# Kernel tuning notes

Measured on AMD Instinct MI355X. Metric: run time of the kernel, lower is better.

The kernel has to match this reference:

```python
import jax, jax.numpy as jnp
import numpy as np

EPS = 1e-8
N, C, R = 512, 32, 32


def _eijk():
    e = np.zeros((3, 3, 3), np.float32)
    e[0, 1, 2] = e[1, 2, 0] = e[2, 0, 1] = 1.0
    e[0, 2, 1] = e[2, 1, 0] = e[1, 0, 2] = -1.0
    return jnp.asarray(e)


def _unit(v):
    # unit_vectors: v / (|v| + EPS)
    return v / (jnp.linalg.norm(v, axis=-1, keepdims=True) + EPS)


def _y2(r):
    # real l=2 spherical harmonics (TFN convention), [N,N,5]
    x, y, z = r[..., 0], r[..., 1], r[..., 2]
    r2 = jnp.maximum(jnp.sum(r * r, axis=-1), EPS)
    c = float(2.0 * np.sqrt(3.0))
    return jnp.stack([
        x * y / r2,
        y * z / r2,
        (-x * x - y * y + 2.0 * z * z) / (c * r2),
        z * x / r2,
        (x * x - y * y) / (2.0 * r2),
    ], axis=-1)


def _forward(in0, in1, in2, rbf, rij,
             w1_f00, b1_f00, w2_f00, b2_f00,
             w1_f01, b1_f01, w2_f01, b2_f01,
             w1_f02, b1_f02, w2_f02, b2_f02,
             w1_f10, b1_f10, w2_f10, b2_f10,
             w1_f11, b1_f11, w2_f11, b2_f11):
    def rad(w1, b1, w2, b2):
        # RadialFunction: relu(b1 + rbf @ w1^T) @ w2^T + b2 -> [N,N,C]
        h = jax.nn.relu(b1 + jnp.einsum('abr,hr->abh', rbf, w1))
        return b2 + jnp.einsum('abh,ch->abc', h, w2)

    # mask self/zero-distance pairs (dij < EPS -> radial = 0), as in F_1/F_2
    mask = (jnp.linalg.norm(rij, axis=-1) >= EPS).astype(rbf.dtype)[..., None]  # [N,N,1]
    u = _unit(rij)    # [N,N,3]
    y2 = _y2(rij)     # [N,N,5]

    r00 = rad(w1_f00, b1_f00, w2_f00, b2_f00)            # scalar filter F_0
    r01 = rad(w1_f01, b1_f01, w2_f01, b2_f01) * mask     # F_1 radial, 0x1->1
    r02 = rad(w1_f02, b1_f02, w2_f02, b2_f02) * mask     # F_2 radial, 0x2->2
    r10 = rad(w1_f10, b1_f10, w2_f10, b2_f10) * mask     # F_1 radial, 1x1->0
    r11 = rad(w1_f11, b1_f11, w2_f11, b2_f11) * mask     # F_1 radial, 1x1->1

    # Filter_0_output_0 (identity CG): L x 0 -> L, aggregate over neighbors b
    o0_s = jnp.einsum('abf,bfi->afi', r00, in0)          # [N,C,1]
    o1_s = jnp.einsum('abf,bfi->afi', r00, in1)          # [N,C,3]
    o2_s = jnp.einsum('abf,bfi->afi', r00, in2)          # [N,C,5]
    o1_a = jnp.einsum('abi,abf,bf->afi', u, r01, in0[..., 0])
    o2_a = jnp.einsum('abi,abf,bf->afi', y2, r02, in0[..., 0])
    o0_b = jnp.einsum('abj,abf,bfj->af', u, r10, in1)[..., None]
    o1_c = jnp.einsum('ijk,abj,abf,bfk->afi', _eijk(), u, r11, in1)

    return (jnp.stack([o0_s, o0_b]),          # [2,N,C,1]
            jnp.stack([o1_a, o1_s, o1_c]),    # [3,N,C,3]
            jnp.stack([o2_a, o2_s]))          # [2,N,C,5]


def setup_inputs() -> dict:
    key = jax.random.key(0)
    ks = jax.random.split(key, 16)

    def xav(k, shape):
        lim = float(np.sqrt(6.0 / (shape[0] + shape[1])))
        return jax.random.uniform(k, shape, jnp.float32, -lim, lim)

    pos = jax.random.normal(ks[0], (N, 3), jnp.float32) * 3.0
    rij = pos[:, None, :] - pos[None, :, :]  # [N,N,3]; zero diagonal exercises the dij<EPS mask
    inp = {
        'in0': jax.random.normal(ks[1], (N, C, 1), jnp.float32),
        'in1': jax.random.normal(ks[2], (N, C, 3), jnp.float32),
        'in2': jax.random.normal(ks[3], (N, C, 5), jnp.float32),
        'rbf': jax.random.uniform(ks[4], (N, N, R), jnp.float32),
        'rij': rij,
    }
    for i, n in enumerate(['f00', 'f01', 'f02', 'f10', 'f11']):
        inp['w1_' + n] = xav(ks[5 + 2 * i], (R, R))
        inp['b1_' + n] = jnp.zeros((R,), jnp.float32)
        inp['w2_' + n] = xav(ks[6 + 2 * i], (C, R))
        inp['b2_' + n] = jnp.zeros((C,), jnp.float32)
    return inp


def reference(in0, in1, in2, rbf, rij,
              w1_f00, b1_f00, w2_f00, b2_f00,
              w1_f01, b1_f01, w2_f01, b2_f01,
              w1_f02, b1_f02, w2_f02, b2_f02,
              w1_f10, b1_f10, w2_f10, b2_f10,
              w1_f11, b1_f11, w2_f11, b2_f11):
    return _forward(in0, in1, in2, rbf, rij,
                    w1_f00, b1_f00, w2_f00, b2_f00,
                    w1_f01, b1_f01, w2_f01, b2_f01,
                    w1_f02, b1_f02, w2_f02, b2_f02,
                    w1_f10, b1_f10, w2_f10, b2_f10,
                    w1_f11, b1_f11, w2_f11, b2_f11)
```

## Files before the change

kernel.cpp:

```cpp
#include <hip/hip_runtime.h>
#include <math.h>

#define NN 512
#define CC 32
#define EPSF 1e-8f
#define WS 40
#define GS 12

typedef __attribute__((ext_vector_type(8))) short bf16x8;
typedef __attribute__((ext_vector_type(4))) float f32x4;

__device__ __forceinline__ short f2bf(float f) {
    unsigned u = __float_as_uint(f);
    u += 0x7fffu + ((u >> 16) & 1u);
    return (short)(u >> 16);
}

__device__ __forceinline__ unsigned cvtpk(float lo, float hi) {
    unsigned r;
    asm("v_cvt_pk_bf16_f32 %0, %1, %2" : "=v"(r) : "v"(lo), "v"(hi));
    return r;
}

#define STAGE_F(F, W1P, W2P)                                                   \
    {                                                                          \
        wlds[(((F) * 2 + 0) * 32 + n0) * WS + k0]      = f2bf((W1P)[tid]);     \
        wlds[(((F) * 2 + 0) * 32 + n0 + 16) * WS + k0] = f2bf((W1P)[tid+512]); \
        wlds[(((F) * 2 + 1) * 32 + n0) * WS + k2]      = f2bf((W2P)[tid]);     \
        wlds[(((F) * 2 + 1) * 32 + n0 + 16) * WS + k2] = f2bf((W2P)[tid+512]); \
    }

#define MLP3S(WOFF, BOFF, B2V, R)                                                  \
    {                                                                              \
        const bf16x8 w1loM = *(const bf16x8*)&wlds[(WOFF) + ln * WS + q * 8];      \
        const bf16x8 w1hiM = *(const bf16x8*)&wlds[(WOFF) + (16 + ln) * WS + q * 8]; \
        f32x4 d0M = *(const f32x4*)&b1lds[(BOFF) + 4 * q];                         \
        f32x4 d1M = *(const f32x4*)&b1lds[(BOFF) + 16 + 4 * q];                    \
        d0M = __builtin_amdgcn_mfma_f32_16x16x32_bf16(w1loM, rbfF, d0M, 0, 0, 0);  \
        d1M = __builtin_amdgcn_mfma_f32_16x16x32_bf16(w1hiM, rbfF, d1M, 0, 0, 0);  \
        union { bf16x8 v; unsigned u[4]; } hu;                                     \
        hu.u[0] = cvtpk(fmaxf(d0M[0], 0.f), fmaxf(d0M[1], 0.f));                   \
        hu.u[1] = cvtpk(fmaxf(d0M[2], 0.f), fmaxf(d0M[3], 0.f));                   \
        hu.u[2] = cvtpk(fmaxf(d1M[0], 0.f), fmaxf(d1M[1], 0.f));                   \
        hu.u[3] = cvtpk(fmaxf(d1M[2], 0.f), fmaxf(d1M[3], 0.f));                   \
        const bf16x8 w2M = *(const bf16x8*)&wlds[(WOFF) + (32 + ch0 + ln) * WS + q * 8]; \
        f32x4 eM = { (B2V), (B2V), (B2V), (B2V) };                                 \
        R = __builtin_amdgcn_mfma_f32_16x16x32_bf16(hu.v, w2M, eM, 0, 0, 0);       \
    }

#define AGGM(RR)                                                               \
    {                                                                          \
        const int bA = b0 + q * 4 + (RR);                                      \
        const f32x4 gA = *(const f32x4*)&geomall[bA][0];                       \
        const f32x4 gB = *(const f32x4*)&geomall[bA][4];                       \
        const float i0A = in0[bA * CC + cw];                                   \
        const float* i1A = in1 + (bA * CC + cw) * 3;                           \
        const float x1A = i1A[0], y1A = i1A[1], z1A = i1A[2];                  \
        const float* i2A = in2 + (bA * CC + cw) * 5;                           \
        const float p0A = i2A[0], p1A = i2A[1], p2A = i2A[2];                  \
        const float p3A = i2A[3], p4A = i2A[4];                                \
        const float s0A = rF0[(RR)];                                           \
        a0  = fmaf(s0A, i0A, a0);                                              \
        a5  = fmaf(s0A, x1A, a5);                                              \
        a6  = fmaf(s0A, y1A, a6);                                              \
        a7  = fmaf(s0A, z1A, a7);                                              \
        a16 = fmaf(s0A, p0A, a16);                                             \
        a17 = fmaf(s0A, p1A, a17);                                             \
        a18 = fmaf(s0A, p2A, a18);                                             \
        a19 = fmaf(s0A, p3A, a19);                                             \
        a20 = fmaf(s0A, p4A, a20);                                             \
        const float t1A = rF1[(RR)] * i0A;                                     \
        a2  = fmaf(t1A, gA[0], a2);                                            \
        a3  = fmaf(t1A, gA[1], a3);                                            \
        a4  = fmaf(t1A, gA[2], a4);                                            \
        const float t2A = rF2[(RR)] * i0A;                                     \
        a11 = fmaf(t2A, gA[3], a11);                                           \
        a12 = fmaf(t2A, gB[0], a12);                                           \
        a13 = fmaf(t2A, gB[1], a13);                                           \
        a14 = fmaf(t2A, gB[2], a14);                                           \
        a15 = fmaf(t2A, gB[3], a15);                                           \
        const float dtA = fmaf(gA[2], z1A, fmaf(gA[1], y1A, gA[0] * x1A));     \
        a1  = fmaf(rF3[(RR)], dtA, a1);                                        \
        const float cxA = fmaf(gA[1], z1A, -(gA[2] * y1A));                    \
        const float cyA = fmaf(gA[2], x1A, -(gA[0] * z1A));                    \
        const float czA = fmaf(gA[0], y1A, -(gA[1] * x1A));                    \
        a8  = fmaf(rF4[(RR)], cxA, a8);                                        \
        a9  = fmaf(rF4[(RR)], cyA, a9);                                        \
        a10 = fmaf(rF4[(RR)], czA, a10);                                       \
    }

#define RED(CMP, V)                                                            \
    {                                                                          \
        float vR = (V);                                                        \
        vR += __shfl_down(vR, 32);                                             \
        vR += __shfl_down(vR, 16);                                             \
        if (lane < 16) red[(w * 21 + (CMP)) * 16 + ln] = vR;                   \
    }

__global__ __launch_bounds__(512, 3) void tfn_mfma(
    const float* __restrict__ in0,
    const float* __restrict__ in1,
    const float* __restrict__ in2,
    const float* __restrict__ rbf,
    const float* __restrict__ rij,
    const float* __restrict__ w1_0, const float* __restrict__ b1_0,
    const float* __restrict__ w2_0, const float* __restrict__ b2_0,
    const float* __restrict__ w1_1, const float* __restrict__ b1_1,
    const float* __restrict__ w2_1, const float* __restrict__ b2_1,
    const float* __restrict__ w1_2, const float* __restrict__ b1_2,
    const float* __restrict__ w2_2, const float* __restrict__ b2_2,
    const float* __restrict__ w1_3, const float* __restrict__ b1_3,
    const float* __restrict__ w2_3, const float* __restrict__ b2_3,
    const float* __restrict__ w1_4, const float* __restrict__ b1_4,
    const float* __restrict__ w2_4, const float* __restrict__ b2_4,
    float* __restrict__ out)
{
    const int a    = blockIdx.x;
    const int tid  = threadIdx.x;
    const int w    = tid >> 6;
    const int lane = tid & 63;
    const int q    = lane >> 4;
    const int ln   = lane & 15;
    const int ch0  = (w & 1) * 16;
    const int cw   = ch0 + ln;

    __shared__ short wlds[5 * 2 * 32 * WS];
    __shared__ float geomall[NN][GS];
    __shared__ float b1lds[5 * 32];

    const int n0 = tid >> 5, k0 = tid & 31;
    const int k2 = (k0 < 16) ? ((k0 >> 2) * 8 + (k0 & 3))
                             : (((k0 - 16) >> 2) * 8 + 4 + ((k0 - 16) & 3));

    STAGE_F(0, w1_0, w2_0)
    STAGE_F(1, w1_1, w2_1)
    STAGE_F(2, w1_2, w2_2)
    STAGE_F(3, w1_3, w2_3)
    STAGE_F(4, w1_4, w2_4)

    if (tid < 32) {
        b1lds[0 * 32 + tid] = b1_0[tid];
        b1lds[1 * 32 + tid] = b1_1[tid];
        b1lds[2 * 32 + tid] = b1_2[tid];
        b1lds[3 * 32 + tid] = b1_3[tid];
        b1lds[4 * 32 + tid] = b1_4[tid];
    }

    const size_t rowbase = (size_t)a * NN;
    const float Y2C = 0.28867513459481287f;

    {
        const float* rp = rij + (rowbase + tid) * 3;
        const float x = rp[0], y = rp[1], z = rp[2];
        const float d2 = x * x + y * y + z * z;
        const float d  = sqrtf(d2);
        const float m  = (d >= EPSF) ? 1.f : 0.f;
        const float inv = m / (d + EPSF);
        const float ir2 = m / fmaxf(d2, EPSF);
        f32x4 gA = { x * inv, y * inv, z * inv, x * y * ir2 };
        f32x4 gB = { y * z * ir2, (2.f * z * z - x * x - y * y) * (ir2 * Y2C),
                     z * x * ir2, (x * x - y * y) * (ir2 * 0.5f) };
        *(f32x4*)&geomall[tid][0] = gA;
        *(f32x4*)&geomall[tid][4] = gB;
    }

    const float b2v0 = b2_0[cw], b2v1 = b2_1[cw], b2v2 = b2_2[cw];
    const float b2v3 = b2_3[cw], b2v4 = b2_4[cw];
    __syncthreads();

    float a0 = 0.f, a1 = 0.f, a2 = 0.f, a3 = 0.f, a4 = 0.f, a5 = 0.f, a6 = 0.f;
    float a7 = 0.f, a8 = 0.f, a9 = 0.f, a10 = 0.f, a11 = 0.f, a12 = 0.f, a13 = 0.f;
    float a14 = 0.f, a15 = 0.f, a16 = 0.f, a17 = 0.f, a18 = 0.f, a19 = 0.f, a20 = 0.f;

    const int pairb = (w >> 1) * 128;
    const float* rbase = rbf + (rowbase + pairb + ln) * 32 + q * 8;

    f32x4 curA = *(const f32x4*)rbase;
    f32x4 curB = *(const f32x4*)(rbase + 4);

    #pragma unroll 1
    for (int t = 0; t < 8; ++t) {
        const int b0 = pairb + t * 16;

        union { bf16x8 v; unsigned u[4]; } ru;
        ru.u[0] = cvtpk(curA[0], curA[1]);
        ru.u[1] = cvtpk(curA[2], curA[3]);
        ru.u[2] = cvtpk(curB[0], curB[1]);
        ru.u[3] = cvtpk(curB[2], curB[3]);
        const bf16x8 rbfF = ru.v;
        if (t < 7) {
            curA = *(const f32x4*)(rbase + (t + 1) * 512);
            curB = *(const f32x4*)(rbase + (t + 1) * 512 + 4);
        }

        f32x4 rF0, rF1, rF2, rF3, rF4;
        MLP3S(0 * 64 * WS, 0 * 32, b2v0, rF0)
        MLP3S(1 * 64 * WS, 1 * 32, b2v1, rF1)
        MLP3S(2 * 64 * WS, 2 * 32, b2v2, rF2)
        MLP3S(3 * 64 * WS, 3 * 32, b2v3, rF3)
        MLP3S(4 * 64 * WS, 4 * 32, b2v4, rF4)

        AGGM(0) AGGM(1) AGGM(2) AGGM(3)
    }

    __syncthreads();
    float* red = (float*)wlds;
    RED(0,  a0)  RED(1,  a1)  RED(2,  a2)  RED(3,  a3)  RED(4,  a4)
    RED(5,  a5)  RED(6,  a6)  RED(7,  a7)  RED(8,  a8)  RED(9,  a9)
    RED(10, a10) RED(11, a11) RED(12, a12) RED(13, a13) RED(14, a14)
    RED(15, a15) RED(16, a16) RED(17, a17) RED(18, a18) RED(19, a19)
    RED(20, a20)
    __syncthreads();

    const int NC = NN * CC;
    for (int e = tid; e < 21 * 32; e += 512) {
        const int cmp = e >> 5, c = e & 31;
        const int hh = c >> 4, l2 = c & 15;
        float s = 0.f;
        #pragma unroll
        for (int p = 0; p < 4; ++p)
            s += red[((p * 2 + hh) * 21 + cmp) * 16 + l2];
        int idx;
        if (cmp == 0)       idx = a * CC + c;
        else if (cmp == 1)  idx = NC + a * CC + c;
        else if (cmp < 5)   idx = 2 * NC + (a * CC + c) * 3 + (cmp - 2);
        else if (cmp < 8)   idx = 2 * NC + 3 * NC + (a * CC + c) * 3 + (cmp - 5);
        else if (cmp < 11)  idx = 2 * NC + 6 * NC + (a * CC + c) * 3 + (cmp - 8);
        else if (cmp < 16)  idx = 11 * NC + (a * CC + c) * 5 + (cmp - 11);
        else                idx = 11 * NC + 5 * NC + (a * CC + c) * 5 + (cmp - 16);
        out[idx] = s;
    }
}

extern "C" void kernel_launch(void* const* d_in, const int* in_sizes, int n_in,
                              void* d_out, int out_size, void* d_ws, size_t ws_size,
                              hipStream_t stream) {
    const float* in0 = (const float*)d_in[0];
    const float* in1 = (const float*)d_in[1];
    const float* in2 = (const float*)d_in[2];
    const float* rbf = (const float*)d_in[3];
    const float* rij = (const float*)d_in[4];

    hipLaunchKernelGGL(tfn_mfma, dim3(NN), dim3(512), 0, stream,
                       in0, in1, in2, rbf, rij,
                       (const float*)d_in[5],  (const float*)d_in[6],
                       (const float*)d_in[7],  (const float*)d_in[8],
                       (const float*)d_in[9],  (const float*)d_in[10],
                       (const float*)d_in[11], (const float*)d_in[12],
                       (const float*)d_in[13], (const float*)d_in[14],
                       (const float*)d_in[15], (const float*)d_in[16],
                       (const float*)d_in[17], (const float*)d_in[18],
                       (const float*)d_in[19], (const float*)d_in[20],
                       (const float*)d_in[21], (const float*)d_in[22],
                       (const float*)d_in[23], (const float*)d_in[24],
                       (float*)d_out);
}
```

Measured before the change: 40.28 us.

## Software-pipeline MFMA radial MLP with aggregation using double-buffered filter registers

Result: slower. 98.15 us (+143.6%).

```diff
diff --git a/kernel.cpp b/kernel.cpp
--- a/kernel.cpp
+++ b/kernel.cpp
@@ -48,7 +48,26 @@
         R = __builtin_amdgcn_mfma_f32_16x16x32_bf16(hu.v, w2M, eM, 0, 0, 0);       \
     }
 
-#define AGGM(RR)                                                               \
+#define MLP_GROUP(NEXT_T, DO_PF, R0, R1, R2, R3, R4)                           \
+    {                                                                          \
+        union { bf16x8 v; unsigned u[4]; } ru;                                 \
+        ru.u[0] = cvtpk(pfA[0], pfA[1]);                                       \
+        ru.u[1] = cvtpk(pfA[2], pfA[3]);                                       \
+        ru.u[2] = cvtpk(pfB[0], pfB[1]);                                       \
+        ru.u[3] = cvtpk(pfB[2], pfB[3]);                                       \
+        const bf16x8 rbfF = ru.v;                                              \
+        if (DO_PF) {                                                           \
+            pfA = *(const f32x4*)(rbase + (NEXT_T) * 512);                     \
+            pfB = *(const f32x4*)(rbase + (NEXT_T) * 512 + 4);                 \
+        }                                                                      \
+        MLP3S(0 * 64 * WS, 0 * 32, b2v0, R0)                                   \
+        MLP3S(1 * 64 * WS, 1 * 32, b2v1, R1)                                   \
+        MLP3S(2 * 64 * WS, 2 * 32, b2v2, R2)                                   \
+        MLP3S(3 * 64 * WS, 3 * 32, b2v3, R3)                                   \
+        MLP3S(4 * 64 * WS, 4 * 32, b2v4, R4)                                   \
+    }
+
+#define AGGM(RR, S0, S1, S2, S3, S4)                                           \
     {                                                                          \
         const int bA = b0 + q * 4 + (RR);                                      \
         const f32x4 gA = *(const f32x4*)&geomall[bA][0];                       \
@@ -59,7 +78,7 @@
         const float* i2A = in2 + (bA * CC + cw) * 5;                           \
         const float p0A = i2A[0], p1A = i2A[1], p2A = i2A[2];                  \
         const float p3A = i2A[3], p4A = i2A[4];                                \
-        const float s0A = rF0[(RR)];                                           \
+        const float s0A = S0[(RR)];                                            \
         a0  = fmaf(s0A, i0A, a0);                                              \
         a5  = fmaf(s0A, x1A, a5);                                              \
         a6  = fmaf(s0A, y1A, a6);                                              \
@@ -69,24 +88,33 @@
         a18 = fmaf(s0A, p2A, a18);                                             \
         a19 = fmaf(s0A, p3A, a19);                                             \
         a20 = fmaf(s0A, p4A, a20);                                             \
-        const float t1A = rF1[(RR)] * i0A;                                     \
+        const float t1A = S1[(RR)] * i0A;                                      \
         a2  = fmaf(t1A, gA[0], a2);                                            \
         a3  = fmaf(t1A, gA[1], a3);                                            \
         a4  = fmaf(t1A, gA[2], a4);                                            \
-        const float t2A = rF2[(RR)] * i0A;                                     \
+        const float t2A = S2[(RR)] * i0A;                                      \
         a11 = fmaf(t2A, gA[3], a11);                                           \
         a12 = fmaf(t2A, gB[0], a12);                                           \
         a13 = fmaf(t2A, gB[1], a13);                                           \
         a14 = fmaf(t2A, gB[2], a14);                                           \
         a15 = fmaf(t2A, gB[3], a15);                                           \
         const float dtA = fmaf(gA[2], z1A, fmaf(gA[1], y1A, gA[0] * x1A));     \
-        a1  = fmaf(rF3[(RR)], dtA, a1);                                        \
+        a1  = fmaf(S3[(RR)], dtA, a1);                                         \
         const float cxA = fmaf(gA[1], z1A, -(gA[2] * y1A));                    \
         const float cyA = fmaf(gA[2], x1A, -(gA[0] * z1A));                    \
         const float czA = fmaf(gA[0], y1A, -(gA[1] * x1A));                    \
-        a8  = fmaf(rF4[(RR)], cxA, a8);                                        \
-        a9  = fmaf(rF4[(RR)], cyA, a9);                                        \
-        a10 = fmaf(rF4[(RR)], czA, a10);                                       \
+        a8  = fmaf(S4[(RR)], cxA, a8);                                         \
+        a9  = fmaf(S4[(RR)], cyA, a9);                                         \
+        a10 = fmaf(S4[(RR)], czA, a10);                                        \
+    }
+
+#define AGGM4(T, S0, S1, S2, S3, S4)                                           \
+    {                                                                          \
+        const int b0 = pairb + (T) * 16;                                       \
+        AGGM(0, S0, S1, S2, S3, S4)                                            \
+        AGGM(1, S0, S1, S2, S3, S4)                                            \
+        AGGM(2, S0, S1, S2, S3, S4)                                            \
+        AGGM(3, S0, S1, S2, S3, S4)                                            \
     }
 
 #define RED(CMP, V)                                                            \
@@ -97,7 +125,7 @@
         if (lane < 16) red[(w * 21 + (CMP)) * 16 + ln] = vR;                   \
     }
 
-__global__ __launch_bounds__(512, 3) void tfn_mfma(
+__global__ __launch_bounds__(512, 2) void tfn_mfma(
     const float* __restrict__ in0,
     const float* __restrict__ in1,
     const float* __restrict__ in2,
@@ -175,33 +203,22 @@
     const int pairb = (w >> 1) * 128;
     const float* rbase = rbf + (rowbase + pairb + ln) * 32 + q * 8;
 
-    f32x4 curA = *(const f32x4*)rbase;
-    f32x4 curB = *(const f32x4*)(rbase + 4);
+    f32x4 pfA = *(const f32x4*)rbase;
+    f32x4 pfB = *(const f32x4*)(rbase + 4);
+    f32x4 rA0, rA1, rA2, rA3, rA4, rB0, rB1, rB2, rB3, rB4;
+
+    MLP_GROUP(1, 1, rA0, rA1, rA2, rA3, rA4)
 
     #pragma unroll 1
-    for (int t = 0; t < 8; ++t) {
-        const int b0 = pairb + t * 16;
-
-        union { bf16x8 v; unsigned u[4]; } ru;
-        ru.u[0] = cvtpk(curA[0], curA[1]);
-        ru.u[1] = cvtpk(curA[2], curA[3]);
-        ru.u[2] = cvtpk(curB[0], curB[1]);
-        ru.u[3] = cvtpk(curB[2], curB[3]);
-        const bf16x8 rbfF = ru.v;
-        if (t < 7) {
-            curA = *(const f32x4*)(rbase + (t + 1) * 512);
-            curB = *(const f32x4*)(rbase + (t + 1) * 512 + 4);
-        }
-
-        f32x4 rF0, rF1, rF2, rF3, rF4;
-        MLP3S(0 * 64 * WS, 0 * 32, b2v0, rF0)
-        MLP3S(1 * 64 * WS, 1 * 32, b2v1, rF1)
-        MLP3S(2 * 64 * WS, 2 * 32, b2v2, rF2)
-        MLP3S(3 * 64 * WS, 3 * 32, b2v3, rF3)
-        MLP3S(4 * 64 * WS, 4 * 32, b2v4, rF4)
-
-        AGGM(0) AGGM(1) AGGM(2) AGGM(3)
-    }
+    for (int tt = 0; tt < 3; ++tt) {
+        MLP_GROUP(2 * tt + 2, 1, rB0, rB1, rB2, rB3, rB4)
+        AGGM4(2 * tt,     rA0, rA1, rA2, rA3, rA4)
+        MLP_GROUP(2 * tt + 3, 1, rA0, rA1, rA2, rA3, rA4)
+        AGGM4(2 * tt + 1, rB0, rB1, rB2, rB3, rB4)
+    }
+    MLP_GROUP(0, 0, rB0, rB1, rB2, rB3, rB4)
+    AGGM4(6, rA0, rA1, rA2, rA3, rA4)
+    AGGM4(7, rB0, rB1, rB2, rB3, rB4)
 
     __syncthreads();
     float* red = (float*)wlds;
```

## Switch radial MLPs to 32x32x16 MFMA covering all channels per wave

Applied to the files above, without the earlier changes.

After: 91.35 us. 2.27x slower.

```diff
diff --git a/kernel.cpp b/kernel.cpp
--- a/kernel.cpp
+++ b/kernel.cpp
@@ -9,6 +9,7 @@
 
 typedef __attribute__((ext_vector_type(8))) short bf16x8;
 typedef __attribute__((ext_vector_type(4))) float f32x4;
+typedef __attribute__((ext_vector_type(16))) float f32x16;
 
 __device__ __forceinline__ short f2bf(float f) {
     unsigned u = __float_as_uint(f);
@@ -30,74 +31,91 @@
         wlds[(((F) * 2 + 1) * 32 + n0 + 16) * WS + k2] = f2bf((W2P)[tid+512]); \
     }
 
-#define MLP3S(WOFF, BOFF, B2V, R)                                                  \
+#define LAYER12(F, B2V, RAD)                                                       \
     {                                                                              \
-        const bf16x8 w1loM = *(const bf16x8*)&wlds[(WOFF) + ln * WS + q * 8];      \
-        const bf16x8 w1hiM = *(const bf16x8*)&wlds[(WOFF) + (16 + ln) * WS + q * 8]; \
-        f32x4 d0M = *(const f32x4*)&b1lds[(BOFF) + 4 * q];                         \
-        f32x4 d1M = *(const f32x4*)&b1lds[(BOFF) + 16 + 4 * q];                    \
-        d0M = __builtin_amdgcn_mfma_f32_16x16x32_bf16(w1loM, rbfF, d0M, 0, 0, 0);  \
-        d1M = __builtin_amdgcn_mfma_f32_16x16x32_bf16(w1hiM, rbfF, d1M, 0, 0, 0);  \
-        union { bf16x8 v; unsigned u[4]; } hu;                                     \
-        hu.u[0] = cvtpk(fmaxf(d0M[0], 0.f), fmaxf(d0M[1], 0.f));                   \
-        hu.u[1] = cvtpk(fmaxf(d0M[2], 0.f), fmaxf(d0M[3], 0.f));                   \
-        hu.u[2] = cvtpk(fmaxf(d1M[0], 0.f), fmaxf(d1M[1], 0.f));                   \
-        hu.u[3] = cvtpk(fmaxf(d1M[2], 0.f), fmaxf(d1M[3], 0.f));                   \
-        const bf16x8 w2M = *(const bf16x8*)&wlds[(WOFF) + (32 + ch0 + ln) * WS + q * 8]; \
-        f32x4 eM = { (B2V), (B2V), (B2V), (B2V) };                                 \
-        R = __builtin_amdgcn_mfma_f32_16x16x32_bf16(hu.v, w2M, eM, 0, 0, 0);       \
-    }
-
-#define AGGM(RR)                                                               \
-    {                                                                          \
-        const int bA = b0 + q * 4 + (RR);                                      \
-        const f32x4 gA = *(const f32x4*)&geomall[bA][0];                       \
-        const f32x4 gB = *(const f32x4*)&geomall[bA][4];                       \
-        const float i0A = in0[bA * CC + cw];                                   \
-        const float* i1A = in1 + (bA * CC + cw) * 3;                           \
-        const float x1A = i1A[0], y1A = i1A[1], z1A = i1A[2];                  \
-        const float* i2A = in2 + (bA * CC + cw) * 5;                           \
-        const float p0A = i2A[0], p1A = i2A[1], p2A = i2A[2];                  \
-        const float p3A = i2A[3], p4A = i2A[4];                                \
-        const float s0A = rF0[(RR)];                                           \
-        a0  = fmaf(s0A, i0A, a0);                                              \
-        a5  = fmaf(s0A, x1A, a5);                                              \
-        a6  = fmaf(s0A, y1A, a6);                                              \
-        a7  = fmaf(s0A, z1A, a7);                                              \
-        a16 = fmaf(s0A, p0A, a16);                                             \
-        a17 = fmaf(s0A, p1A, a17);                                             \
-        a18 = fmaf(s0A, p2A, a18);                                             \
-        a19 = fmaf(s0A, p3A, a19);                                             \
-        a20 = fmaf(s0A, p4A, a20);                                             \
-        const float t1A = rF1[(RR)] * i0A;                                     \
+        const bf16x8 w1i0M = *(const bf16x8*)&wlds[(((F)*2+0)*32 + cc)*WS + 8*hp]; \
+        const bf16x8 w1i1M = *(const bf16x8*)&wlds[(((F)*2+0)*32 + cc)*WS + 16 + 8*hp]; \
+        f32x16 d1M = *(const f32x16*)&b1p[(F)*32 + hp*16];                         \
+        d1M = __builtin_amdgcn_mfma_f32_32x32x16_bf16(w1i0M, rbf0F, d1M, 0, 0, 0); \
+        d1M = __builtin_amdgcn_mfma_f32_32x32x16_bf16(w1i1M, rbf1F, d1M, 0, 0, 0); \
+        union { bf16x8 v; unsigned u[4]; } hAM, hBM;                               \
+        hAM.u[0] = cvtpk(fmaxf(d1M[0],  0.f), fmaxf(d1M[1],  0.f));                \
+        hAM.u[1] = cvtpk(fmaxf(d1M[2],  0.f), fmaxf(d1M[3],  0.f));                \
+        hAM.u[2] = cvtpk(fmaxf(d1M[4],  0.f), fmaxf(d1M[5],  0.f));                \
+        hAM.u[3] = cvtpk(fmaxf(d1M[6],  0.f), fmaxf(d1M[7],  0.f));                \
+        hBM.u[0] = cvtpk(fmaxf(d1M[8],  0.f), fmaxf(d1M[9],  0.f));                \
+        hBM.u[1] = cvtpk(fmaxf(d1M[10], 0.f), fmaxf(d1M[11], 0.f));                \
+        hBM.u[2] = cvtpk(fmaxf(d1M[12], 0.f), fmaxf(d1M[13], 0.f));                \
+        hBM.u[3] = cvtpk(fmaxf(d1M[14], 0.f), fmaxf(d1M[15], 0.f));                \
+        const bf16x8 w2i0M = *(const bf16x8*)&wlds[(((F)*2+1)*32 + cc)*WS + 8*hp]; \
+        const bf16x8 w2i1M = *(const bf16x8*)&wlds[(((F)*2+1)*32 + cc)*WS + 16 + 8*hp]; \
+        f32x16 rdM = { (B2V),(B2V),(B2V),(B2V),(B2V),(B2V),(B2V),(B2V),            \
+                       (B2V),(B2V),(B2V),(B2V),(B2V),(B2V),(B2V),(B2V) };          \
+        rdM = __builtin_amdgcn_mfma_f32_32x32x16_bf16(hAM.v, w2i0M, rdM, 0, 0, 0); \
+        rdM = __builtin_amdgcn_mfma_f32_32x32x16_bf16(hBM.v, w2i1M, rdM, 0, 0, 0); \
+        RAD = rdM;                                                                 \
+    }
+
+#define POFF(R) (((R) & 3) + 8 * ((R) >> 2))
+
+#define AGG0R(R)                                                               \
+    {                                                                          \
+        const float sA = rad0[(R)];                                            \
+        const float i0A = p0b[POFF(R) * 32];                                   \
+        const float xA = p1b[POFF(R)*96 + 0], yA = p1b[POFF(R)*96 + 1], zA = p1b[POFF(R)*96 + 2]; \
+        a0  = fmaf(sA, i0A, a0);                                               \
+        a5  = fmaf(sA, xA, a5);                                                \
+        a6  = fmaf(sA, yA, a6);                                                \
+        a7  = fmaf(sA, zA, a7);                                                \
+        a16 = fmaf(sA, p2b[POFF(R)*160 + 0], a16);                             \
+        a17 = fmaf(sA, p2b[POFF(R)*160 + 1], a17);                             \
+        a18 = fmaf(sA, p2b[POFF(R)*160 + 2], a18);                             \
+        a19 = fmaf(sA, p2b[POFF(R)*160 + 3], a19);                             \
+        a20 = fmaf(sA, p2b[POFF(R)*160 + 4], a20);                             \
+    }
+
+#define AGG12R(R)                                                              \
+    {                                                                          \
+        const f32x4 gA = *(const f32x4*)&geomall[gbb + POFF(R)][0];            \
+        const f32x4 gB = *(const f32x4*)&geomall[gbb + POFF(R)][4];            \
+        const float i0A = p0b[POFF(R) * 32];                                   \
+        const float t1A = rad1[(R)] * i0A;                                     \
         a2  = fmaf(t1A, gA[0], a2);                                            \
         a3  = fmaf(t1A, gA[1], a3);                                            \
         a4  = fmaf(t1A, gA[2], a4);                                            \
-        const float t2A = rF2[(RR)] * i0A;                                     \
+        const float t2A = rad2[(R)] * i0A;                                     \
         a11 = fmaf(t2A, gA[3], a11);                                           \
         a12 = fmaf(t2A, gB[0], a12);                                           \
         a13 = fmaf(t2A, gB[1], a13);                                           \
         a14 = fmaf(t2A, gB[2], a14);                                           \
         a15 = fmaf(t2A, gB[3], a15);                                           \
-        const float dtA = fmaf(gA[2], z1A, fmaf(gA[1], y1A, gA[0] * x1A));     \
-        a1  = fmaf(rF3[(RR)], dtA, a1);                                        \
-        const float cxA = fmaf(gA[1], z1A, -(gA[2] * y1A));                    \
-        const float cyA = fmaf(gA[2], x1A, -(gA[0] * z1A));                    \
-        const float czA = fmaf(gA[0], y1A, -(gA[1] * x1A));                    \
-        a8  = fmaf(rF4[(RR)], cxA, a8);                                        \
-        a9  = fmaf(rF4[(RR)], cyA, a9);                                        \
-        a10 = fmaf(rF4[(RR)], czA, a10);                                       \
-    }
+    }
+
+#define AGG34R(R)                                                              \
+    {                                                                          \
+        const f32x4 gA = *(const f32x4*)&geomall[gbb + POFF(R)][0];            \
+        const float xA = p1b[POFF(R)*96 + 0], yA = p1b[POFF(R)*96 + 1], zA = p1b[POFF(R)*96 + 2]; \
+        const float dtA = fmaf(gA[2], zA, fmaf(gA[1], yA, gA[0] * xA));        \
+        a1  = fmaf(rad3[(R)], dtA, a1);                                        \
+        const float cxA = fmaf(gA[1], zA, -(gA[2] * yA));                      \
+        const float cyA = fmaf(gA[2], xA, -(gA[0] * zA));                      \
+        const float czA = fmaf(gA[0], yA, -(gA[1] * xA));                      \
+        a8  = fmaf(rad4[(R)], cxA, a8);                                        \
+        a9  = fmaf(rad4[(R)], cyA, a9);                                        \
+        a10 = fmaf(rad4[(R)], czA, a10);                                       \
+    }
+
+#define AGG16(M) M(0) M(1) M(2) M(3) M(4) M(5) M(6) M(7) \
+                 M(8) M(9) M(10) M(11) M(12) M(13) M(14) M(15)
 
 #define RED(CMP, V)                                                            \
     {                                                                          \
         float vR = (V);                                                        \
         vR += __shfl_down(vR, 32);                                             \
-        vR += __shfl_down(vR, 16);                                             \
-        if (lane < 16) red[(w * 21 + (CMP)) * 16 + ln] = vR;                   \
-    }
-
-__global__ __launch_bounds__(512, 3) void tfn_mfma(
+        if (lane < 32) red[(w * 21 + (CMP)) * 32 + lane] = vR;                 \
+    }
+
+__global__ __launch_bounds__(512, 2) void tfn_mfma(
     const float* __restrict__ in0,
     const float* __restrict__ in1,
     const float* __restrict__ in2,
@@ -119,18 +137,16 @@
     const int tid  = threadIdx.x;
     const int w    = tid >> 6;
     const int lane = tid & 63;
-    const int q    = lane >> 4;
-    const int ln   = lane & 15;
-    const int ch0  = (w & 1) * 16;
-    const int cw   = ch0 + ln;
+    const int cc   = lane & 31;
+    const int hp   = lane >> 5;
 
     __shared__ short wlds[5 * 2 * 32 * WS];
     __shared__ float geomall[NN][GS];
-    __shared__ float b1lds[5 * 32];
+    __shared__ float b1p[5 * 32];
 
     const int n0 = tid >> 5, k0 = tid & 31;
-    const int k2 = (k0 < 16) ? ((k0 >> 2) * 8 + (k0 & 3))
-                             : (((k0 - 16) >> 2) * 8 + 4 + ((k0 - 16) & 3));
+    const int np_ = k0 & 15;
+    const int k2 = (k0 >> 4) * 16 + ((np_ >> 2) & 1) * 8 + (np_ & 3) + 4 * (np_ >> 3);
 
     STAGE_F(0, w1_0, w2_0)
     STAGE_F(1, w1_1, w2_1)
@@ -139,11 +155,13 @@
     STAGE_F(4, w1_4, w2_4)
 
     if (tid < 32) {
-        b1lds[0 * 32 + tid] = b1_0[tid];
-        b1lds[1 * 32 + tid] = b1_1[tid];
-        b1lds[2 * 32 + tid] = b1_2[tid];
-        b1lds[3 * 32 + tid] = b1_3[tid];
-        b1lds[4 * 32 + tid] = b1_4[tid];
+        const int rr_ = tid & 15, hh_ = tid >> 4;
+        const int ns_ = (rr_ & 3) + 8 * (rr_ >> 2) + 4 * hh_;
+        b1p[0 * 32 + tid] = b1_0[ns_];
+        b1p[1 * 32 + tid] = b1_1[ns_];
+        b1p[2 * 32 + tid] = b1_2[ns_];
+        b1p[3 * 32 + tid] = b1_3[ns_];
+        b1p[4 * 32 + tid] = b1_4[ns_];
     }
 
     const size_t rowbase = (size_t)a * NN;
@@ -164,43 +182,54 @@
         *(f32x4*)&geomall[tid][4] = gB;
     }
 
-    const float b2v0 = b2_0[cw], b2v1 = b2_1[cw], b2v2 = b2_2[cw];
-    const float b2v3 = b2_3[cw], b2v4 = b2_4[cw];
+    const float b2v0 = b2_0[cc], b2v1 = b2_1[cc], b2v2 = b2_2[cc];
+    const float b2v3 = b2_3[cc], b2v4 = b2_4[cc];
     __syncthreads();
 
     float a0 = 0.f, a1 = 0.f, a2 = 0.f, a3 = 0.f, a4 = 0.f, a5 = 0.f, a6 = 0.f;
     float a7 = 0.f, a8 = 0.f, a9 = 0.f, a10 = 0.f, a11 = 0.f, a12 = 0.f, a13 = 0.f;
     float a14 = 0.f, a15 = 0.f, a16 = 0.f, a17 = 0.f, a18 = 0.f, a19 = 0.f, a20 = 0.f;
 
-    const int pairb = (w >> 1) * 128;
-    const float* rbase = rbf + (rowbase + pairb + ln) * 32 + q * 8;
-
-    f32x4 curA = *(const f32x4*)rbase;
-    f32x4 curB = *(const f32x4*)(rbase + 4);
+    const float* rb_base = rbf + (rowbase + w * 64 + cc) * 32;
+    f32x4 pA0 = *(const f32x4*)(rb_base + 8 * hp);
+    f32x4 pA1 = *(const f32x4*)(rb_base + 8 * hp + 4);
+    f32x4 pB0 = *(const f32x4*)(rb_base + 16 + 8 * hp);
+    f32x4 pB1 = *(const f32x4*)(rb_base + 16 + 8 * hp + 4);
 
     #pragma unroll 1
-    for (int t = 0; t < 8; ++t) {
-        const int b0 = pairb + t * 16;
-
-        union { bf16x8 v; unsigned u[4]; } ru;
-        ru.u[0] = cvtpk(curA[0], curA[1]);
-        ru.u[1] = cvtpk(curA[2], curA[3]);
-        ru.u[2] = cvtpk(curB[0], curB[1]);
-        ru.u[3] = cvtpk(curB[2], curB[3]);
-        const bf16x8 rbfF = ru.v;
-        if (t < 7) {
-            curA = *(const f32x4*)(rbase + (t + 1) * 512);
-            curB = *(const f32x4*)(rbase + (t + 1) * 512 + 4);
+    for (int T = 0; T < 2; ++T) {
+        const int b0  = w * 64 + T * 32;
+        const int gbb = b0 + 4 * hp;
+        const float* p0b = in0 + gbb * CC + cc;
+        const float* p1b = in1 + (gbb * CC + cc) * 3;
+        const float* p2b = in2 + (gbb * CC + cc) * 5;
+
+        union { bf16x8 v; unsigned u[4]; } r0u, r1u;
+        r0u.u[0] = cvtpk(pA0[0], pA0[1]); r0u.u[1] = cvtpk(pA0[2], pA0[3]);
+        r0u.u[2] = cvtpk(pA1[0], pA1[1]); r0u.u[3] = cvtpk(pA1[2], pA1[3]);
+        r1u.u[0] = cvtpk(pB0[0], pB0[1]); r1u.u[1] = cvtpk(pB0[2], pB0[3]);
+        r1u.u[2] = cvtpk(pB1[0], pB1[1]); r1u.u[3] = cvtpk(pB1[2], pB1[3]);
+        const bf16x8 rbf0F = r0u.v;
+        const bf16x8 rbf1F = r1u.v;
+        if (T == 0) {
+            pA0 = *(const f32x4*)(rb_base + 1024 + 8 * hp);
+            pA1 = *(const f32x4*)(rb_base + 1024 + 8 * hp + 4);
+            pB0 = *(const f32x4*)(rb_base + 1024 + 16 + 8 * hp);
+            pB1 = *(const f32x4*)(rb_base + 1024 + 16 + 8 * hp + 4);
         }
 
-        f32x4 rF0, rF1, rF2, rF3, rF4;
-        MLP3S(0 * 64 * WS, 0 * 32, b2v0, rF0)
-        MLP3S(1 * 64 * WS, 1 * 32, b2v1, rF1)
-        MLP3S(2 * 64 * WS, 2 * 32, b2v2, rF2)
-        MLP3S(3 * 64 * WS, 3 * 32, b2v3, rF3)
-        MLP3S(4 * 64 * WS, 4 * 32, b2v4, rF4)
-
-        AGGM(0) AGGM(1) AGGM(2) AGGM(3)
+        f32x16 rad0, rad1, rad2, rad3, rad4;
+
+        LAYER12(0, b2v0, rad0)
+        AGG16(AGG0R)
+
+        LAYER12(1, b2v1, rad1)
+        LAYER12(2, b2v2, rad2)
+        AGG16(AGG12R)
+
+        LAYER12(3, b2v3, rad3)
+        LAYER12(4, b2v4, rad4)
+        AGG16(AGG34R)
     }
 
     __syncthreads();
@@ -215,11 +244,9 @@
     const int NC = NN * CC;
     for (int e = tid; e < 21 * 32; e += 512) {
         const int cmp = e >> 5, c = e & 31;
-        const int hh = c >> 4, l2 = c & 15;
         float s = 0.f;
         #pragma unroll
-        for (int p = 0; p < 4; ++p)
-            s += red[((p * 2 + hh) * 21 + cmp) * 16 + l2];
+        for (int g = 0; g < 8; ++g) s += red[(g * 21 + cmp) * 32 + c];
         int idx;
         if (cmp == 0)       idx = a * CC + c;
         else if (cmp == 1)  idx = NC + a * CC + c;
```
